# Performance work log

Hardware: AMD Instinct MI355X
Metric: run time of the kernel (lower is better)

## Reference

```python
import jax, jax.numpy as jnp
import numpy as np

N_COG = 72  # 360 / delta_cog
N_RB = 72   # 360 / delta_rb
B, N, H = 64, 512, 128


def setup_inputs() -> dict:
    key = jax.random.key(0)
    k1, k2, k3, k4, k5, k6 = jax.random.split(key, 6)
    h_t = jax.random.normal(k1, (N, B, H), dtype=jnp.float32)
    r_mat = jax.random.randint(k2, (B, N, N), 0, N_RB, dtype=jnp.int32)
    d_mat = jax.random.uniform(k3, (B, N, N), dtype=jnp.float32)
    mask = jax.random.randint(k4, (B, N), 0, 2).astype(jnp.float32)
    cog_mat = jax.random.randint(k5, (B, N, N), 0, N_COG, dtype=jnp.int32)
    domain = jax.random.normal(k6, (N_COG, N_RB), dtype=jnp.float32)
    return {"h_t": h_t, "r_mat": r_mat, "d_mat": d_mat, "mask": mask,
            "cog_mat": cog_mat, "domain": domain}


def reference(h_t, r_mat, d_mat, mask, cog_mat, domain):
    # gather from learnable domain table, subtract distance, relu
    w = jax.nn.relu(domain[cog_mat, r_mat] - d_mat)          # [B, N, N]
    # pairwise mask (applied twice in the original, around normalization)
    m = mask[:, :, None] * mask[:, None, :]                   # [B, N, N]
    w = m * w
    # global-max normalize; torch uses .data.max() (no grad through max)
    w = w / jax.lax.stop_gradient(jnp.max(w))
    w = m * w
    # out[b,i,h] = sum_j w[b,i,j] * h_t[j,b,h]
    return jnp.einsum('bij,jbh->bih', w, h_t)                 # [B, N, H]
```

## Files before the change

### kernel.cpp

```cpp
#include <hip/hip_runtime.h>


#define B_   64
#define N_   512
#define H_   128
#define NCOG 72
#define NRB  72

typedef __bf16 bf16x8 __attribute__((ext_vector_type(8)));
typedef float  f32x4  __attribute__((ext_vector_type(4)));
typedef unsigned int u32x4 __attribute__((ext_vector_type(4)));

__global__ __launch_bounds__(256) void k_transpose(const float* __restrict__ ht,
                                                   __bf16* __restrict__ T) {
    __shared__ __bf16 tile[32][136];
    const int jt = blockIdx.x * 32;
    const int b  = blockIdx.y;
    const int t  = threadIdx.x;
    {
        const int jj = t >> 3;
        const int h0 = (t & 7) << 4;
        const float* src = ht + ((size_t)(jt + jj) * B_ + b) * H_ + h0;
        float4 v0 = *(const float4*)(src + 0);
        float4 v1 = *(const float4*)(src + 4);
        float4 v2 = *(const float4*)(src + 8);
        float4 v3 = *(const float4*)(src + 12);
        __bf16* dst = &tile[jj][h0];
        dst[0]=(__bf16)v0.x; dst[1]=(__bf16)v0.y; dst[2]=(__bf16)v0.z; dst[3]=(__bf16)v0.w;
        dst[4]=(__bf16)v1.x; dst[5]=(__bf16)v1.y; dst[6]=(__bf16)v1.z; dst[7]=(__bf16)v1.w;
        dst[8]=(__bf16)v2.x; dst[9]=(__bf16)v2.y; dst[10]=(__bf16)v2.z; dst[11]=(__bf16)v2.w;
        dst[12]=(__bf16)v3.x; dst[13]=(__bf16)v3.y; dst[14]=(__bf16)v3.z; dst[15]=(__bf16)v3.w;
    }
    __syncthreads();
    {
        const int h  = t >> 1;
        const int j0 = (t & 1) << 4;
        union { bf16x8 v[2]; __bf16 e[16]; } ob;
        #pragma unroll
        for (int q = 0; q < 16; ++q) ob.e[q] = tile[j0 + q][h];
        __bf16* dst = T + ((size_t)b * H_ + h) * N_ + jt + j0;
        *(bf16x8*)(dst + 0) = ob.v[0];
        *(bf16x8*)(dst + 8) = ob.v[1];
    }
}

__global__ __launch_bounds__(512) void k_main(const int* __restrict__ cog,
                                              const int* __restrict__ rmat,
                                              const float* __restrict__ dmat,
                                              const float* __restrict__ mask,
                                              const float* __restrict__ domain,
                                              const __bf16* __restrict__ T,
                                              float* __restrict__ out,
                                              unsigned int* __restrict__ gmax) {
    __shared__ int   tiles[2 * 3 * 2048];
    __shared__ float sdom[NCOG * NRB];
    __shared__ float smask[N_];
    __shared__ float swmax[8];

    const int id    = blockIdx.x;
    const int xcd   = id & 7;
    const int i0idx = (id >> 3) & 7;
    const int bhi   = id >> 6;
    const int b     = xcd + 8 * bhi;
    const int i0    = i0idx * 64;
    const int kstart = (id & 15) * 32;

    const int t    = threadIdx.x;
    const int wave = t >> 6;
    const int lane = t & 63;

    for (int k = t; k < NCOG * NRB; k += 512) sdom[k] = domain[k];
    for (int k = t; k < N_; k += 512) smask[k] = mask[b * N_ + k];

    const size_t robase = ((size_t)b * N_ + i0) * N_;

    float wmax = 0.0f;

    if (wave >= 4) {
        const int pw = wave - 4;
        const int r  = lane >> 3;
        const int c  = lane & 7;
        const size_t gl_off = (size_t)r * N_ + c * 4;
        const int    ds_off = r * 32 + ((c ^ r) << 2);

        u32x4 regs[2][6];

        #define LOAD_BATCH(n, set)                                                   \
            do {                                                                     \
                const int kk_ = (kstart + (n) * 32) & (N_ - 1);                      \
                _Pragma("unroll")                                                    \
                for (int q6 = 0; q6 < 6; ++q6) {                                     \
                    const int q = pw * 6 + q6, a = q >> 3, c8 = q & 7;               \
                    const size_t goff = robase + (size_t)(c8 * 8) * N_ + kk_ + gl_off;\
                    const unsigned int* g = (a == 0) ? (const unsigned int*)cog      \
                                           : (a == 1) ? (const unsigned int*)rmat    \
                                                      : (const unsigned int*)dmat;   \
                    regs[set][q6] = __builtin_nontemporal_load((const u32x4*)(g + goff)); \
                }                                                                    \
            } while (0)

        #define STORE_BATCH(n, set)                                                  \
            do {                                                                     \
                const int buf_ = (n) & 1;                                            \
                _Pragma("unroll")                                                    \
                for (int q6 = 0; q6 < 6; ++q6) {                                     \
                    const int q = pw * 6 + q6, a = q >> 3, c8 = q & 7;               \
                    *(u32x4*)&tiles[buf_ * 6144 + a * 2048 + c8 * 256 + ds_off] = regs[set][q6]; \
                }                                                                    \
            } while (0)

        LOAD_BATCH(0, 0);
        LOAD_BATCH(1, 1);
        STORE_BATCH(0, 0);
        asm volatile("s_waitcnt lgkmcnt(0)\n\ts_barrier" ::: "memory");

        #pragma unroll
        for (int s = 0; s < 16; ++s) {
            if (s < 14) LOAD_BATCH(s + 2, s & 1);
            __builtin_amdgcn_sched_barrier(0);
            if (s < 15) STORE_BATCH(s + 1, (s + 1) & 1);
            asm volatile("s_waitcnt lgkmcnt(0)\n\ts_barrier" ::: "memory");
        }
        #undef LOAD_BATCH
        #undef STORE_BATCH
    } else {
        const int quad = lane >> 4;
        const int lrow = lane & 15;
        const int row  = wave * 16 + lrow;
        const int g0   = (row * 8 + ((quad * 2)     ^ (row & 7))) * 4;
        const int g1   = (row * 8 + ((quad * 2 + 1) ^ (row & 7))) * 4;
        const __bf16* Tcol = T + (size_t)b * H_ * N_ + (size_t)lrow * N_ + quad * 8;

        f32x4 acc[8];
        #pragma unroll
        for (int i = 0; i < 8; ++i) acc[i] = (f32x4)0.0f;

        __syncthreads();
        #pragma unroll 4
        for (int s = 0; s < 16; ++s) {
            const int kk  = (kstart + s * 32) & (N_ - 1);
            bf16x8 bfbuf[8];
            #pragma unroll
            for (int nt = 0; nt < 8; ++nt)
                bfbuf[nt] = *(const bf16x8*)(Tcol + (size_t)nt * 16 * N_ + kk);
            const int jb = kk + quad * 8;
            const int* tb = tiles + (s & 1) * 6144;
            union { int4 v[2]; int   e[8]; } ci, ri;
            union { int4 v[2]; float e[8]; } di;
            ci.v[0] = *(const int4*)(tb + g0);        ci.v[1] = *(const int4*)(tb + g1);
            ri.v[0] = *(const int4*)(tb + 2048 + g0); ri.v[1] = *(const int4*)(tb + 2048 + g1);
            di.v[0] = *(const int4*)(tb + 4096 + g0); di.v[1] = *(const int4*)(tb + 4096 + g1);

            union { bf16x8 v8; __bf16 e[8]; } af;
            #pragma unroll
            for (int q = 0; q < 8; ++q) {
                float val = sdom[ci.e[q] * NRB + ri.e[q]] - di.e[q];
                val = fmaxf(val, 0.0f) * smask[jb + q];
                wmax = fmaxf(wmax, val);
                af.e[q] = (__bf16)val;
            }
            #pragma unroll
            for (int nt = 0; nt < 8; ++nt)
                acc[nt] = __builtin_amdgcn_mfma_f32_16x16x32_bf16(af.v8, bfbuf[nt], acc[nt], 0, 0, 0);
            __syncthreads();
        }

        wmax *= smask[i0 + row];

        const int orow0 = i0 + wave * 16 + quad * 4;
        #pragma unroll
        for (int nt = 0; nt < 8; ++nt) {
            #pragma unroll
            for (int r = 0; r < 4; ++r)
                out[((size_t)b * N_ + orow0 + r) * H_ + nt * 16 + lrow] = acc[nt][r];
        }
    }

    #pragma unroll
    for (int off = 32; off > 0; off >>= 1)
        wmax = fmaxf(wmax, __shfl_down(wmax, off));
    if (lane == 0) swmax[wave] = wmax;
    __syncthreads();
    if (t == 0) {
        float m = swmax[0];
        #pragma unroll
        for (int w = 1; w < 8; ++w) m = fmaxf(m, swmax[w]);
        atomicMax(gmax, __float_as_uint(m));
    }
}

__global__ __launch_bounds__(256) void k_scale(float* __restrict__ out,
                                               const float* __restrict__ mask,
                                               const unsigned int* __restrict__ gmax) {
    const float inv = 1.0f / __uint_as_float(*gmax);
    const int idx = blockIdx.x * 256 + threadIdx.x;
    const float m = mask[idx >> 5] * inv;
    float4* p = (float4*)out;
    float4 v = p[idx];
    v.x *= m; v.y *= m; v.z *= m; v.w *= m;
    p[idx] = v;
}

extern "C" void kernel_launch(void* const* d_in, const int* in_sizes, int n_in,
                              void* d_out, int out_size, void* d_ws, size_t ws_size,
                              hipStream_t stream) {
    const float* ht     = (const float*)d_in[0];
    const int*   rmat   = (const int*)  d_in[1];
    const float* dmat   = (const float*)d_in[2];
    const float* mask   = (const float*)d_in[3];
    const int*   cog    = (const int*)  d_in[4];
    const float* domain = (const float*)d_in[5];
    float* out = (float*)d_out;

    unsigned int* gmax = (unsigned int*)d_ws;
    __bf16* T = (__bf16*)((char*)d_ws + 256);

    hipMemsetAsync(d_ws, 0, 256, stream);
    k_transpose<<<dim3(16, 64), 256, 0, stream>>>(ht, T);
    k_main<<<dim3(512), 512, 0, stream>>>(cog, rmat, dmat, mask, domain, T, out, gmax);
    k_scale<<<4096, 256, 0, stream>>>(out, mask, gmax);
}
```

Before: 227.1 us.

## Producer waves compute bf16 weight tiles into LDS; consumers MFMA with two-tile overlap

```diff
diff --git a/kernel.cpp b/kernel.cpp
--- a/kernel.cpp
+++ b/kernel.cpp
@@ -8,6 +8,7 @@
 #define NRB  72
 
 typedef __bf16 bf16x8 __attribute__((ext_vector_type(8)));
+typedef __bf16 bf16x4 __attribute__((ext_vector_type(4)));
 typedef float  f32x4  __attribute__((ext_vector_type(4)));
 typedef unsigned int u32x4 __attribute__((ext_vector_type(4)));
 
@@ -52,18 +53,14 @@
                                               const __bf16* __restrict__ T,
                                               float* __restrict__ out,
                                               unsigned int* __restrict__ gmax) {
-    __shared__ int   tiles[2 * 3 * 2048];
-    __shared__ float sdom[NCOG * NRB];
-    __shared__ float smask[N_];
-    __shared__ float swmax[8];
-
-    const int id    = blockIdx.x;
-    const int xcd   = id & 7;
-    const int i0idx = (id >> 3) & 7;
-    const int bhi   = id >> 6;
-    const int b     = xcd + 8 * bhi;
-    const int i0    = i0idx * 64;
-    const int kstart = (id & 15) * 32;
+    __shared__ __bf16 wt[2][64][512];
+    __shared__ float  sdom[NCOG * NRB];
+    __shared__ float  smask[N_];
+    __shared__ float  swmax[8];
+
+    const int id   = blockIdx.x;
+    const int b    = (id & 7) + 8 * (id >> 5);
+    const int pair = (id >> 3) & 3;
 
     const int t    = threadIdx.x;
     const int wave = t >> 6;
@@ -72,109 +69,95 @@
     for (int k = t; k < NCOG * NRB; k += 512) sdom[k] = domain[k];
     for (int k = t; k < N_; k += 512) smask[k] = mask[b * N_ + k];
 
-    const size_t robase = ((size_t)b * N_ + i0) * N_;
-
     float wmax = 0.0f;
 
-    if (wave >= 4) {
-        const int pw = wave - 4;
-        const int r  = lane >> 3;
-        const int c  = lane & 7;
-        const size_t gl_off = (size_t)r * N_ + c * 4;
-        const int    ds_off = r * 32 + ((c ^ r) << 2);
-
-        u32x4 regs[2][6];
-
-        #define LOAD_BATCH(n, set)                                                   \
+    const int pw = wave - 4;
+    auto FILL = [&](int tile) {
+        const int i0_t = pair * 128 + tile * 64;
+        const size_t rowbase0 = ((size_t)b * N_ + i0_t + pw * 16) * N_ + lane * 4;
+        const f32x4 mj0 = *(const f32x4*)&smask[lane * 4];
+        const f32x4 mj1 = *(const f32x4*)&smask[256 + lane * 4];
+
+        u32x4 rc[2][2], rr[2][2];
+        f32x4 rd[2][2];
+
+        #define PLOAD(u, set)                                                        \
             do {                                                                     \
-                const int kk_ = (kstart + (n) * 32) & (N_ - 1);                      \
-                _Pragma("unroll")                                                    \
-                for (int q6 = 0; q6 < 6; ++q6) {                                     \
-                    const int q = pw * 6 + q6, a = q >> 3, c8 = q & 7;               \
-                    const size_t goff = robase + (size_t)(c8 * 8) * N_ + kk_ + gl_off;\
-                    const unsigned int* g = (a == 0) ? (const unsigned int*)cog      \
-                                           : (a == 1) ? (const unsigned int*)rmat    \
-                                                      : (const unsigned int*)dmat;   \
-                    regs[set][q6] = __builtin_nontemporal_load((const u32x4*)(g + goff)); \
-                }                                                                    \
+                const size_t rb_ = rowbase0 + (size_t)(u) * N_;                      \
+                rc[set][0] = __builtin_nontemporal_load((const u32x4*)((const unsigned int*)cog + rb_));        \
+                rc[set][1] = __builtin_nontemporal_load((const u32x4*)((const unsigned int*)cog + rb_ + 256));  \
+                rr[set][0] = __builtin_nontemporal_load((const u32x4*)((const unsigned int*)rmat + rb_));       \
+                rr[set][1] = __builtin_nontemporal_load((const u32x4*)((const unsigned int*)rmat + rb_ + 256)); \
+                rd[set][0] = __builtin_nontemporal_load((const f32x4*)(dmat + rb_));         \
+                rd[set][1] = __builtin_nontemporal_load((const f32x4*)(dmat + rb_ + 256));   \
             } while (0)
 
-        #define STORE_BATCH(n, set)                                                  \
-            do {                                                                     \
-                const int buf_ = (n) & 1;                                            \
-                _Pragma("unroll")                                                    \
-                for (int q6 = 0; q6 < 6; ++q6) {                                     \
-                    const int q = pw * 6 + q6, a = q >> 3, c8 = q & 7;               \
-                    *(u32x4*)&tiles[buf_ * 6144 + a * 2048 + c8 * 256 + ds_off] = regs[set][q6]; \
-                }                                                                    \
-            } while (0)
-
-        LOAD_BATCH(0, 0);
-        LOAD_BATCH(1, 1);
-        STORE_BATCH(0, 0);
-        asm volatile("s_waitcnt lgkmcnt(0)\n\ts_barrier" ::: "memory");
-
-        #pragma unroll
-        for (int s = 0; s < 16; ++s) {
-            if (s < 14) LOAD_BATCH(s + 2, s & 1);
+        PLOAD(0, 0);
+        #pragma unroll
+        for (int u = 0; u < 16; ++u) {
+            if (u < 15) PLOAD(u + 1, (u + 1) & 1);
             __builtin_amdgcn_sched_barrier(0);
-            if (s < 15) STORE_BATCH(s + 1, (s + 1) & 1);
-            asm volatile("s_waitcnt lgkmcnt(0)\n\ts_barrier" ::: "memory");
+            const int set = u & 1;
+            const int rl  = pw * 16 + u;
+            const float mi = smask[i0_t + rl];
+            const int swz  = (rl & 7) << 4;
+            char* wrow = (char*)&wt[tile & 1][rl][0];
+            bf16x4 pa, pb;
+            #pragma unroll
+            for (int q = 0; q < 4; ++q) {
+                float v0 = sdom[rc[set][0][q] * NRB + rr[set][0][q]] - rd[set][0][q];
+                v0 = fmaxf(v0, 0.0f) * mj0[q] * mi;
+                wmax = fmaxf(wmax, v0);
+                pa[q] = (__bf16)v0;
+                float v1 = sdom[rc[set][1][q] * NRB + rr[set][1][q]] - rd[set][1][q];
+                v1 = fmaxf(v1, 0.0f) * mj1[q] * mi;
+                wmax = fmaxf(wmax, v1);
+                pb[q] = (__bf16)v1;
+            }
+            *(bf16x4*)(wrow + ((lane * 8) ^ swz))       = pa;
+            *(bf16x4*)(wrow + ((lane * 8 + 512) ^ swz)) = pb;
         }
-        #undef LOAD_BATCH
-        #undef STORE_BATCH
-    } else {
-        const int quad = lane >> 4;
-        const int lrow = lane & 15;
-        const int row  = wave * 16 + lrow;
-        const int g0   = (row * 8 + ((quad * 2)     ^ (row & 7))) * 4;
-        const int g1   = (row * 8 + ((quad * 2 + 1) ^ (row & 7))) * 4;
-        const __bf16* Tcol = T + (size_t)b * H_ * N_ + (size_t)lrow * N_ + quad * 8;
-
+        #undef PLOAD
+    };
+
+    const int quad = lane >> 4;
+    const int lrow = lane & 15;
+    const __bf16* Tcol = T + (size_t)b * H_ * N_ + (size_t)lrow * N_ + quad * 8;
+    auto COMPUTE = [&](int tile) {
+        const int i0_t  = pair * 128 + tile * 64;
+        const int row_l = wave * 16 + lrow;
+        const char* wrow = (const char*)&wt[tile & 1][row_l][0];
+        const int swz = (row_l & 7) << 4;
         f32x4 acc[8];
         #pragma unroll
         for (int i = 0; i < 8; ++i) acc[i] = (f32x4)0.0f;
-
-        __syncthreads();
         #pragma unroll 4
         for (int s = 0; s < 16; ++s) {
-            const int kk  = (kstart + s * 32) & (N_ - 1);
-            bf16x8 bfbuf[8];
+            const int kk = s * 32;
+            bf16x8 bfb[8];
             #pragma unroll
             for (int nt = 0; nt < 8; ++nt)
-                bfbuf[nt] = *(const bf16x8*)(Tcol + (size_t)nt * 16 * N_ + kk);
-            const int jb = kk + quad * 8;
-            const int* tb = tiles + (s & 1) * 6144;
-            union { int4 v[2]; int   e[8]; } ci, ri;
-            union { int4 v[2]; float e[8]; } di;
-            ci.v[0] = *(const int4*)(tb + g0);        ci.v[1] = *(const int4*)(tb + g1);
-            ri.v[0] = *(const int4*)(tb + 2048 + g0); ri.v[1] = *(const int4*)(tb + 2048 + g1);
-            di.v[0] = *(const int4*)(tb + 4096 + g0); di.v[1] = *(const int4*)(tb + 4096 + g1);
-
-            union { bf16x8 v8; __bf16 e[8]; } af;
-            #pragma unroll
-            for (int q = 0; q < 8; ++q) {
-                float val = sdom[ci.e[q] * NRB + ri.e[q]] - di.e[q];
-                val = fmaxf(val, 0.0f) * smask[jb + q];
-                wmax = fmaxf(wmax, val);
-                af.e[q] = (__bf16)val;
-            }
+                bfb[nt] = *(const bf16x8*)(Tcol + nt * 16 * N_ + kk);
+            const bf16x8 af = *(const bf16x8*)(wrow + ((kk * 2 + quad * 16) ^ swz));
             #pragma unroll
             for (int nt = 0; nt < 8; ++nt)
-                acc[nt] = __builtin_amdgcn_mfma_f32_16x16x32_bf16(af.v8, bfbuf[nt], acc[nt], 0, 0, 0);
-            __syncthreads();
+                acc[nt] = __builtin_amdgcn_mfma_f32_16x16x32_bf16(af, bfb[nt], acc[nt], 0, 0, 0);
         }
-
-        wmax *= smask[i0 + row];
-
-        const int orow0 = i0 + wave * 16 + quad * 4;
+        const int orow0 = i0_t + wave * 16 + quad * 4;
         #pragma unroll
         for (int nt = 0; nt < 8; ++nt) {
             #pragma unroll
             for (int r = 0; r < 4; ++r)
                 out[((size_t)b * N_ + orow0 + r) * H_ + nt * 16 + lrow] = acc[nt][r];
         }
-    }
+    };
+
+    __syncthreads();
+    if (wave >= 4) FILL(0);
+    __syncthreads();
+    if (wave >= 4) FILL(1); else COMPUTE(0);
+    __syncthreads();
+    if (wave < 4) COMPUTE(1);
 
     #pragma unroll
     for (int off = 32; off > 0; off >>= 1)
@@ -190,14 +173,12 @@
 }
 
 __global__ __launch_bounds__(256) void k_scale(float* __restrict__ out,
-                                               const float* __restrict__ mask,
                                                const unsigned int* __restrict__ gmax) {
     const float inv = 1.0f / __uint_as_float(*gmax);
     const int idx = blockIdx.x * 256 + threadIdx.x;
-    const float m = mask[idx >> 5] * inv;
     float4* p = (float4*)out;
     float4 v = p[idx];
-    v.x *= m; v.y *= m; v.z *= m; v.w *= m;
+    v.x *= inv; v.y *= inv; v.z *= inv; v.w *= inv;
     p[idx] = v;
 }
 
@@ -217,6 +198,6 @@
 
     hipMemsetAsync(d_ws, 0, 256, stream);
     k_transpose<<<dim3(16, 64), 256, 0, stream>>>(ht, T);
-    k_main<<<dim3(512), 512, 0, stream>>>(cog, rmat, dmat, mask, domain, T, out, gmax);
-    k_scale<<<4096, 256, 0, stream>>>(out, mask, gmax);
-}
+    k_main<<<dim3(256), 512, 0, stream>>>(cog, rmat, dmat, mask, domain, T, out, gmax);
+    k_scale<<<4096, 256, 0, stream>>>(out, gmax);
+}
```

Measured after the change: 235.1 us. 1.04x slower.
